# Kernel tuning notes

Hardware: AMD Instinct MI355X
Metric: run time of the kernel (lower is better)

Reference implementation:

```python
import jax, jax.numpy as jnp
import numpy as np

NR = 512      # num robots
NT = 1024     # num tasks
E = 500000    # num edges
D = 64        # robot_dim == task_dim (forced by torch.cat dim=0)
ED = 32       # edge_dim
GH = 128      # gnn_hidden
MH = 128      # mlp_hidden
SLOPE = 0.1   # LeakyReLU negative slope


def lrelu(x):
    return jnp.where(x >= 0, x, SLOPE * x)


def _linear(key, out_d, in_d):
    k1, k2 = jax.random.split(key)
    s = 1.0 / np.sqrt(in_d)
    W = jax.random.uniform(k1, (out_d, in_d), minval=-s, maxval=s, dtype=jnp.float32)
    b = jax.random.uniform(k2, (out_d,), minval=-s, maxval=s, dtype=jnp.float32)
    return W, b


def setup_inputs() -> dict:
    key = jax.random.key(0)
    ks = jax.random.split(key, 12)
    x_robot = jax.random.normal(ks[0], (NR, D), dtype=jnp.float32)
    x_task = jax.random.normal(ks[1], (NT, D), dtype=jnp.float32)
    edge_attr = jax.random.normal(ks[2], (E, ED), dtype=jnp.float32)
    src = jax.random.randint(ks[3], (E,), 0, NR)
    tgt = jax.random.randint(ks[4], (E,), 0, NT)
    edge_index = jnp.stack([src, tgt], axis=0).astype(jnp.int64)
    We1, be1 = _linear(ks[5], GH, 2 * D + ED)   # f_theta_e layer 1
    We2, be2 = _linear(ks[6], GH, GH)            # f_theta_e layer 2
    Wv1, bv1 = _linear(ks[7], GH, D + GH)        # f_theta_v layer 1
    Wv2, bv2 = _linear(ks[8], GH, GH)            # f_theta_v layer 2
    Wm1, bm1 = _linear(ks[9], MH, GH + D)        # task selector layer 1
    Wm2, bm2 = _linear(ks[10], 1, MH)            # task selector layer 2
    return {
        'x_robot': x_robot, 'x_task': x_task, 'edge_index': edge_index,
        'edge_attr': edge_attr,
        'We1': We1, 'be1': be1, 'We2': We2, 'be2': be2,
        'Wv1': Wv1, 'bv1': bv1, 'Wv2': Wv2, 'bv2': bv2,
        'Wm1': Wm1, 'bm1': bm1, 'Wm2': Wm2, 'bm2': bm2,
    }


def reference(x_robot, x_task, edge_index, edge_attr,
              We1, be1, We2, be2, Wv1, bv1, Wv2, bv2, Wm1, bm1, Wm2, bm2):
    n_robot = x_robot.shape[0]
    x = jnp.concatenate([x_robot, x_task], axis=0)          # [NR+NT, D]
    src = edge_index[0]                                      # robot indices
    tgt = edge_index[1] + n_robot                            # shifted task indices
    # PyG default flow='source_to_target': x_i = x[target], x_j = x[source],
    # messages are scatter-added at target slots (the task slots here).
    msg_in = jnp.concatenate([x[tgt], x[src], edge_attr], axis=1)  # [E, 2D+ED]
    m = lrelu(msg_in @ We1.T + be1) @ We2.T + be2            # [E, GH]
    agg = jax.ops.segment_sum(m, tgt, num_segments=n_robot + x_task.shape[0])
    robot_msgs = agg[:n_robot]                               # all zeros (faithful to source)
    upd_in = jnp.concatenate([robot_msgs, x_robot], axis=1)  # [NR, GH+D]
    h = lrelu(upd_in @ Wv1.T + bv1) @ Wv2.T + bv2            # [NR, GH]
    # Pairwise MLP on concat([h_i, task_j]) without materializing the concat:
    # split Wm1 columns into the robot-hidden and task parts.
    hr = h @ Wm1[:, :GH].T                                   # [NR, MH]
    ht = x_task @ Wm1[:, GH:].T                              # [NT, MH]
    hid = lrelu(hr[:, None, :] + ht[None, :, :] + bm1)       # [NR, NT, MH]
    scores = jnp.einsum('nmh,h->nm', hid, Wm2[0]) + bm2[0]   # [NR, NT]
    return jax.nn.softmax(scores, axis=1)
```

## Files before the change

kernel.cpp:

```cpp
#include <hip/hip_runtime.h>

#define NRB 512
#define NTK 1024
#define DD  64
#define GHH 128



__global__ __launch_bounds__(256) void task_prep_kernel(
    const float* __restrict__ xt,
    const float* __restrict__ Wm1, const float* __restrict__ bm1,
    const float* __restrict__ Wm2, const float* __restrict__ bm2,
    float* __restrict__ HTBt4, float* __restrict__ cv)
{
    const int t = threadIdx.x;
    const int b = blockIdx.x;
    const int i = t & 127;
    const int g = t >> 7;

    __shared__ float lds_w[128 * 132];
    __shared__ float xs[8 * 64];
    __shared__ float sT[8 * 132];
    __shared__ float sR[8 * 132];

    float4* Lw = reinterpret_cast<float4*>(lds_w);

    const int t0 = b * 8;
    xs[t]       = xt[t0 * DD + t];
    xs[256 + t] = xt[t0 * DD + 256 + t];

    {
        const float4* W = reinterpret_cast<const float4*>(Wm1);
        #pragma unroll
        for (int j = 0; j < 8; ++j) {
            const int e = t + 256 * j;
            const int row = e >> 4, c4 = e & 15;
            Lw[row * 33 + c4] = W[row * 48 + 32 + c4];
        }
    }
    __syncthreads();

    {
        const float bb  = bm1[i];
        const float wm2 = Wm2[i];
        float a0 = bb, a1 = bb, a2 = bb, a3 = bb;
        const float4* w4 = Lw + i * 33;
        const float4* x0 = reinterpret_cast<const float4*>(xs + (4*g)*64);
        const float4* x1 = reinterpret_cast<const float4*>(xs + (4*g+1)*64);
        const float4* x2 = reinterpret_cast<const float4*>(xs + (4*g+2)*64);
        const float4* x3 = reinterpret_cast<const float4*>(xs + (4*g+3)*64);
        #pragma unroll
        for (int k = 0; k < 16; ++k) {
            const float4 w = w4[k];
            const float4 p0 = x0[k], p1 = x1[k], p2 = x2[k], p3 = x3[k];
            a0 = fmaf(w.x, p0.x, a0); a1 = fmaf(w.x, p1.x, a1);
            a2 = fmaf(w.x, p2.x, a2); a3 = fmaf(w.x, p3.x, a3);
            a0 = fmaf(w.y, p0.y, a0); a1 = fmaf(w.y, p1.y, a1);
            a2 = fmaf(w.y, p2.y, a2); a3 = fmaf(w.y, p3.y, a3);
            a0 = fmaf(w.z, p0.z, a0); a1 = fmaf(w.z, p1.z, a1);
            a2 = fmaf(w.z, p2.z, a2); a3 = fmaf(w.z, p3.z, a3);
            a0 = fmaf(w.w, p0.w, a0); a1 = fmaf(w.w, p1.w, a1);
            a2 = fmaf(w.w, p2.w, a2); a3 = fmaf(w.w, p3.w, a3);
        }
        sT[(4*g)*132 + i]   = a0;  sR[(4*g)*132 + i]   = wm2 * a0;
        sT[(4*g+1)*132 + i] = a1;  sR[(4*g+1)*132 + i] = wm2 * a1;
        sT[(4*g+2)*132 + i] = a2;  sR[(4*g+2)*132 + i] = wm2 * a2;
        sT[(4*g+3)*132 + i] = a3;  sR[(4*g+3)*132 + i] = wm2 * a3;
    }
    __syncthreads();

    {
        const int h4 = t >> 3, tk = t & 7;
        float4 v;
        v.x = sT[tk*132 + 4*h4 + 0];
        v.y = sT[tk*132 + 4*h4 + 1];
        v.z = sT[tk*132 + 4*h4 + 2];
        v.w = sT[tk*132 + 4*h4 + 3];
        reinterpret_cast<float4*>(HTBt4)[h4 * NTK + t0 + tk] = v;
    }

    {
        const int row = t >> 5, c = t & 31;
        float s = sR[row*132 + c]      + sR[row*132 + c + 32]
                + sR[row*132 + c + 64] + sR[row*132 + c + 96];
        #pragma unroll
        for (int off = 16; off >= 1; off >>= 1)
            s += __shfl_xor(s, off, 32);
        if (c == 0) cv[t0 + row] = 0.55f * s + bm2[0];
    }
}

__global__ __launch_bounds__(1024) void robot_score_softmax_kernel(
    const float* __restrict__ xr,
    const float* __restrict__ Wv1, const float* __restrict__ bv1,
    const float* __restrict__ Wv2, const float* __restrict__ bv2,
    const float* __restrict__ Wm1, const float* __restrict__ Wm2,
    const float* __restrict__ HTBt4, const float* __restrict__ cv,
    float* __restrict__ out)
{
    const int b   = blockIdx.x;
    const int tid = threadIdx.x;
    const int n0  = b * 2;

    __shared__ float lds_w[128 * 132];
    __shared__ float xs[2 * 64];
    __shared__ float sA[2 * 132];
    __shared__ float sB[2 * 132];
    __shared__ float sR[2 * 132];
    __shared__ float s_hr[2 * 128];
    __shared__ float s_wb[128];
    __shared__ float s_av[2];

    float4* Lw = reinterpret_cast<float4*>(lds_w);

    const float cm = cv[tid];

    if (tid < 128) xs[tid] = xr[n0 * DD + tid];

    {
        const float4* W = reinterpret_cast<const float4*>(Wv1);
        #pragma unroll
        for (int j = 0; j < 2; ++j) {
            const int e = tid + 1024 * j;
            const int row = e >> 4, c4 = e & 15;
            Lw[row * 33 + c4] = W[row * 48 + 32 + c4];
        }
    }
    __syncthreads();

    if (tid < 256) {
        const int i = tid & 127, r = tid >> 7;
        float acc = bv1[i];
        const float4* w4 = Lw + i * 33;
        const float4* x4 = reinterpret_cast<const float4*>(xs + r * 64);
        #pragma unroll
        for (int k = 0; k < 16; ++k) {
            const float4 w = w4[k];
            const float4 p = x4[k];
            acc = fmaf(w.x, p.x, acc);
            acc = fmaf(w.y, p.y, acc);
            acc = fmaf(w.z, p.z, acc);
            acc = fmaf(w.w, p.w, acc);
        }
        sA[r*132 + i] = (acc >= 0.f) ? acc : 0.1f * acc;
    }
    __syncthreads();

    {
        const float4* W = reinterpret_cast<const float4*>(Wv2);
        #pragma unroll
        for (int j = 0; j < 4; ++j) {
            const int e = tid + 1024 * j;
            const int row = e >> 5, c4 = e & 31;
            Lw[row * 33 + c4] = W[row * 32 + c4];
        }
    }
    __syncthreads();

    if (tid < 256) {
        const int i = tid & 127, r = tid >> 7;
        float acc = bv2[i];
        const float4* w4 = Lw + i * 33;
        const float4* h4 = reinterpret_cast<const float4*>(sA + r * 132);
        #pragma unroll 8
        for (int k = 0; k < 32; ++k) {
            const float4 w = w4[k];
            const float4 p = h4[k];
            acc = fmaf(w.x, p.x, acc);
            acc = fmaf(w.y, p.y, acc);
            acc = fmaf(w.z, p.z, acc);
            acc = fmaf(w.w, p.w, acc);
        }
        sB[r*132 + i] = acc;
    }
    __syncthreads();

    {
        const float4* W = reinterpret_cast<const float4*>(Wm1);
        #pragma unroll
        for (int j = 0; j < 4; ++j) {
            const int e = tid + 1024 * j;
            const int row = e >> 5, c4 = e & 31;
            Lw[row * 33 + c4] = W[row * 48 + c4];
        }
        if (tid < 128) s_wb[tid] = 0.45f * Wm2[tid];
    }
    __syncthreads();

    if (tid < 256) {
        const int i = tid & 127, r = tid >> 7;
        float acc = 0.f;
        const float4* w4 = Lw + i * 33;
        const float4* h4 = reinterpret_cast<const float4*>(sB + r * 132);
        #pragma unroll 8
        for (int k = 0; k < 32; ++k) {
            const float4 w = w4[k];
            const float4 p = h4[k];
            acc = fmaf(w.x, p.x, acc);
            acc = fmaf(w.y, p.y, acc);
            acc = fmaf(w.z, p.z, acc);
            acc = fmaf(w.w, p.w, acc);
        }
        s_hr[r*128 + i] = acc;
        sR[r*132 + i]   = Wm2[i] * acc;
    }
    __syncthreads();

    if (tid < 128) {
        const int w = tid >> 6, l = tid & 63;
        float s = sR[w*132 + l] + sR[w*132 + l + 64];
        #pragma unroll
        for (int off = 32; off >= 1; off >>= 1)
            s += __shfl_xor(s, off, 64);
        if (l == 0) s_av[w] = 0.55f * s;
    }
    __syncthreads();

    const float4* tb  = reinterpret_cast<const float4*>(HTBt4) + tid;
    const float4* hrA = reinterpret_cast<const float4*>(s_hr);
    const float4* hrB = reinterpret_cast<const float4*>(s_hr + 128);
    const float4* wb4 = reinterpret_cast<const float4*>(s_wb);

    float acc0 = 0.f, acc1 = 0.f;

    #pragma unroll 4
    for (int h4 = 0; h4 < 32; ++h4) {
        const float4 v  = tb[h4 << 10];
        const float4 w  = wb4[h4];
        const float4 r0 = hrA[h4];
        const float4 r1 = hrB[h4];
        acc0 = fmaf(w.x, fabsf(r0.x + v.x), acc0);
        acc1 = fmaf(w.x, fabsf(r1.x + v.x), acc1);
        acc0 = fmaf(w.y, fabsf(r0.y + v.y), acc0);
        acc1 = fmaf(w.y, fabsf(r1.y + v.y), acc1);
        acc0 = fmaf(w.z, fabsf(r0.z + v.z), acc0);
        acc1 = fmaf(w.z, fabsf(r1.z + v.z), acc1);
        acc0 = fmaf(w.w, fabsf(r0.w + v.w), acc0);
        acc1 = fmaf(w.w, fabsf(r1.w + v.w), acc1);
    }

    float sc[2];
    sc[0] = acc0 + s_av[0] + cm;
    sc[1] = acc1 + s_av[1] + cm;

    __shared__ float rmax[2][16], rsum[2][16];
    const int wid = tid >> 6, lane = tid & 63;

    #pragma unroll
    for (int n = 0; n < 2; ++n) {
        float mx = sc[n];
        #pragma unroll
        for (int off = 32; off >= 1; off >>= 1)
            mx = fmaxf(mx, __shfl_xor(mx, off, 64));
        if (lane == 0) rmax[n][wid] = mx;
    }
    __syncthreads();

    float ex[2];
    #pragma unroll
    for (int n = 0; n < 2; ++n) {
        float mx = rmax[n][0];
        #pragma unroll
        for (int k = 1; k < 16; ++k) mx = fmaxf(mx, rmax[n][k]);
        float e = expf(sc[n] - mx);
        ex[n] = e;
        float s = e;
        #pragma unroll
        for (int off = 32; off >= 1; off >>= 1) s += __shfl_xor(s, off, 64);
        if (lane == 0) rsum[n][wid] = s;
    }
    __syncthreads();

    #pragma unroll
    for (int n = 0; n < 2; ++n) {
        float s = rsum[n][0];
        #pragma unroll
        for (int k = 1; k < 16; ++k) s += rsum[n][k];
        out[(n0 + n) * NTK + tid] = ex[n] * (1.0f / s);
    }
}

extern "C" void kernel_launch(void* const* d_in, const int* in_sizes, int n_in,
                              void* d_out, int out_size, void* d_ws, size_t ws_size,
                              hipStream_t stream)
{
    const float* xr  = (const float*)d_in[0];
    const float* xt  = (const float*)d_in[1];
    const float* Wv1 = (const float*)d_in[8];
    const float* bv1 = (const float*)d_in[9];
    const float* Wv2 = (const float*)d_in[10];
    const float* bv2 = (const float*)d_in[11];
    const float* Wm1 = (const float*)d_in[12];
    const float* bm1 = (const float*)d_in[13];
    const float* Wm2 = (const float*)d_in[14];
    const float* bm2 = (const float*)d_in[15];

    float* ws    = (float*)d_ws;
    float* HTBt4 = ws;
    float* cv    = ws + 131072;
    float* out   = (float*)d_out;

    hipLaunchKernelGGL(task_prep_kernel, dim3(128), dim3(256), 0, stream,
                       xt, Wm1, bm1, Wm2, bm2, HTBt4, cv);
    hipLaunchKernelGGL(robot_score_softmax_kernel, dim3(256), dim3(1024), 0, stream,
                       xr, Wv1, bv1, Wv2, bv2, Wm1, Wm2, HTBt4, cv, out);
}
```

Baseline: 24.42 us.

## Compute robot MLP matvecs with wave-parallel shuffle reductions instead of LDS-staged weights

The robot MLP chain (Wv1, Wv2, Wm1 matvecs) no longer stages each 128x128 weight matrix into a large LDS tile before computing with only 256 of 1024 threads. Each wave now reads weight rows directly from global memory with coalesced loads, multiplies them by the two robots' inputs, and reduces across lanes with xor shuffles, so all 16 waves contribute. This removes the large shared buffer and several weight-copy barriers, aiming to cut serial latency in the per-block prologue and to raise occupancy. The trade-off is more shuffle work and repeated global reads of the weights by every block, which depend on cache hits.

Measured after the change: 35.42 us. 1.45x slower.

```diff
diff --git a/kernel.cpp b/kernel.cpp
--- a/kernel.cpp
+++ b/kernel.cpp
@@ -101,119 +101,107 @@
     const int b   = blockIdx.x;
     const int tid = threadIdx.x;
     const int n0  = b * 2;
-
-    __shared__ float lds_w[128 * 132];
-    __shared__ float xs[2 * 64];
-    __shared__ float sA[2 * 132];
-    __shared__ float sB[2 * 132];
-    __shared__ float sR[2 * 132];
-    __shared__ float s_hr[2 * 128];
-    __shared__ float s_wb[128];
-    __shared__ float s_av[2];
-
-    float4* Lw = reinterpret_cast<float4*>(lds_w);
+    const int wv  = tid >> 6;
+    const int ln  = tid & 63;
+
+    __shared__ __align__(16) float xs[2][64];
+    __shared__ __align__(16) float h1[2][128];
+    __shared__ __align__(16) float hh[2][128];
+    __shared__ __align__(16) float s_hr[2 * 128];
+    __shared__ __align__(16) float s_pr[2 * 128];
+    __shared__ __align__(16) float s_wb[128];
+    __shared__ float s_av[2], s_pp[2][2];
 
     const float cm = cv[tid];
 
-    if (tid < 128) xs[tid] = xr[n0 * DD + tid];
-
-    {
-        const float4* W = reinterpret_cast<const float4*>(Wv1);
-        #pragma unroll
-        for (int j = 0; j < 2; ++j) {
-            const int e = tid + 1024 * j;
-            const int row = e >> 4, c4 = e & 15;
-            Lw[row * 33 + c4] = W[row * 48 + 32 + c4];
+    if (tid < 128) {
+        xs[tid >> 6][tid & 63] = xr[n0 * DD + tid];
+        s_wb[tid] = 0.45f * Wm2[tid];
+    }
+    __syncthreads();
+
+    {
+        const float x0 = xs[0][ln];
+        const float x1 = xs[1][ln];
+        #pragma unroll
+        for (int p = 0; p < 8; ++p) {
+            const int i = p * 16 + wv;
+            const float w = Wv1[i * 192 + 128 + ln];
+            float p0 = w * x0;
+            float p1 = w * x1;
+            #pragma unroll
+            for (int off = 32; off >= 1; off >>= 1) {
+                p0 += __shfl_xor(p0, off, 64);
+                p1 += __shfl_xor(p1, off, 64);
+            }
+            if (ln == 0) {
+                const float bb = bv1[i];
+                float a0 = p0 + bb, a1 = p1 + bb;
+                h1[0][i] = (a0 >= 0.f) ? a0 : 0.1f * a0;
+                h1[1][i] = (a1 >= 0.f) ? a1 : 0.1f * a1;
+            }
+        }
+    }
+    __syncthreads();
+
+    {
+        const float ha0 = h1[0][ln], hb0 = h1[0][64 + ln];
+        const float ha1 = h1[1][ln], hb1 = h1[1][64 + ln];
+        #pragma unroll
+        for (int p = 0; p < 8; ++p) {
+            const int i = p * 16 + wv;
+            const float wa = Wv2[i * 128 + ln];
+            const float wb = Wv2[i * 128 + 64 + ln];
+            float p0 = fmaf(wa, ha0, wb * hb0);
+            float p1 = fmaf(wa, ha1, wb * hb1);
+            #pragma unroll
+            for (int off = 32; off >= 1; off >>= 1) {
+                p0 += __shfl_xor(p0, off, 64);
+                p1 += __shfl_xor(p1, off, 64);
+            }
+            if (ln == 0) {
+                const float bb = bv2[i];
+                hh[0][i] = p0 + bb;
+                hh[1][i] = p1 + bb;
+            }
+        }
+    }
+    __syncthreads();
+
+    {
+        const float ha0 = hh[0][ln], hb0 = hh[0][64 + ln];
+        const float ha1 = hh[1][ln], hb1 = hh[1][64 + ln];
+        #pragma unroll
+        for (int p = 0; p < 8; ++p) {
+            const int i = p * 16 + wv;
+            const float wa = Wm1[i * 192 + ln];
+            const float wb = Wm1[i * 192 + 64 + ln];
+            float p0 = fmaf(wa, ha0, wb * hb0);
+            float p1 = fmaf(wa, ha1, wb * hb1);
+            #pragma unroll
+            for (int off = 32; off >= 1; off >>= 1) {
+                p0 += __shfl_xor(p0, off, 64);
+                p1 += __shfl_xor(p1, off, 64);
+            }
+            if (ln == 0) {
+                const float wm2 = Wm2[i];
+                s_hr[i]       = p0;  s_pr[i]       = wm2 * p0;
+                s_hr[128 + i] = p1;  s_pr[128 + i] = wm2 * p1;
+            }
         }
     }
     __syncthreads();
 
     if (tid < 256) {
-        const int i = tid & 127, r = tid >> 7;
-        float acc = bv1[i];
-        const float4* w4 = Lw + i * 33;
-        const float4* x4 = reinterpret_cast<const float4*>(xs + r * 64);
-        #pragma unroll
-        for (int k = 0; k < 16; ++k) {
-            const float4 w = w4[k];
-            const float4 p = x4[k];
-            acc = fmaf(w.x, p.x, acc);
-            acc = fmaf(w.y, p.y, acc);
-            acc = fmaf(w.z, p.z, acc);
-            acc = fmaf(w.w, p.w, acc);
-        }
-        sA[r*132 + i] = (acc >= 0.f) ? acc : 0.1f * acc;
-    }
-    __syncthreads();
-
-    {
-        const float4* W = reinterpret_cast<const float4*>(Wv2);
-        #pragma unroll
-        for (int j = 0; j < 4; ++j) {
-            const int e = tid + 1024 * j;
-            const int row = e >> 5, c4 = e & 31;
-            Lw[row * 33 + c4] = W[row * 32 + c4];
-        }
-    }
-    __syncthreads();
-
-    if (tid < 256) {
-        const int i = tid & 127, r = tid >> 7;
-        float acc = bv2[i];
-        const float4* w4 = Lw + i * 33;
-        const float4* h4 = reinterpret_cast<const float4*>(sA + r * 132);
-        #pragma unroll 8
-        for (int k = 0; k < 32; ++k) {
-            const float4 w = w4[k];
-            const float4 p = h4[k];
-            acc = fmaf(w.x, p.x, acc);
-            acc = fmaf(w.y, p.y, acc);
-            acc = fmaf(w.z, p.z, acc);
-            acc = fmaf(w.w, p.w, acc);
-        }
-        sB[r*132 + i] = acc;
-    }
-    __syncthreads();
-
-    {
-        const float4* W = reinterpret_cast<const float4*>(Wm1);
-        #pragma unroll
-        for (int j = 0; j < 4; ++j) {
-            const int e = tid + 1024 * j;
-            const int row = e >> 5, c4 = e & 31;
-            Lw[row * 33 + c4] = W[row * 48 + c4];
-        }
-        if (tid < 128) s_wb[tid] = 0.45f * Wm2[tid];
-    }
-    __syncthreads();
-
-    if (tid < 256) {
-        const int i = tid & 127, r = tid >> 7;
-        float acc = 0.f;
-        const float4* w4 = Lw + i * 33;
-        const float4* h4 = reinterpret_cast<const float4*>(sB + r * 132);
-        #pragma unroll 8
-        for (int k = 0; k < 32; ++k) {
-            const float4 w = w4[k];
-            const float4 p = h4[k];
-            acc = fmaf(w.x, p.x, acc);
-            acc = fmaf(w.y, p.y, acc);
-            acc = fmaf(w.z, p.z, acc);
-            acc = fmaf(w.w, p.w, acc);
-        }
-        s_hr[r*128 + i] = acc;
-        sR[r*132 + i]   = Wm2[i] * acc;
-    }
-    __syncthreads();
-
-    if (tid < 128) {
-        const int w = tid >> 6, l = tid & 63;
-        float s = sR[w*132 + l] + sR[w*132 + l + 64];
+        const int r = tid >> 7, c = tid & 127;
+        float s = s_pr[r * 128 + c];
         #pragma unroll
         for (int off = 32; off >= 1; off >>= 1)
             s += __shfl_xor(s, off, 64);
-        if (l == 0) s_av[w] = 0.55f * s;
-    }
+        if ((c & 63) == 0) s_pp[r][c >> 6] = s;
+    }
+    __syncthreads();
+    if (tid < 2) s_av[tid] = 0.55f * (s_pp[tid][0] + s_pp[tid][1]);
     __syncthreads();
 
     const float4* tb  = reinterpret_cast<const float4*>(HTBt4) + tid;
@@ -244,7 +232,7 @@
     sc[1] = acc1 + s_av[1] + cm;
 
     __shared__ float rmax[2][16], rsum[2][16];
-    const int wid = tid >> 6, lane = tid & 63;
+    const int lane = ln;
 
     #pragma unroll
     for (int n = 0; n < 2; ++n) {
@@ -252,7 +240,7 @@
         #pragma unroll
         for (int off = 32; off >= 1; off >>= 1)
             mx = fmaxf(mx, __shfl_xor(mx, off, 64));
-        if (lane == 0) rmax[n][wid] = mx;
+        if (lane == 0) rmax[n][wv] = mx;
     }
     __syncthreads();
 
@@ -267,7 +255,7 @@
         float s = e;
         #pragma unroll
         for (int off = 32; off >= 1; off >>= 1) s += __shfl_xor(s, off, 64);
-        if (lane == 0) rsum[n][wid] = s;
+        if (lane == 0) rsum[n][wv] = s;
     }
     __syncthreads();
 
```
